# Kernel optimization log

Hardware: AMD Instinct MI355X
Metric: run time of the kernel (lower is better)

Reference implementation:

```python
import jax, jax.numpy as jnp
import numpy as np
from jax import lax

# SLAYER neuron / simulation constants (netParams)
THETA = 1.0      # spike threshold
TAU_SR = 4.0     # PSP (SRM) kernel time constant
TAU_REF = 1.0    # refractory kernel time constant
SCALE_REF = 2.0  # refractory scale (kernel amplitude = -scaleRef*theta)
TAU_RHO = 1.0    # surrogate-gradient width (used in bwd only)
SCALE_RHO = 1.0

B, F_IN, T = 8, 6300, 500  # 6300 = 50*63*2
HID, OUT = 32, 20


def _alpha_scan(x, d):
    """Causal conv with alpha kernel k*d**k along last (time) axis via 2-state recurrence.
    x: [..., T]. y[t] = sum_{j<=t} x[j]*(t-j)*d**(t-j)."""
    xt = jnp.moveaxis(x, -1, 0)  # [T, ...]
    zero = jnp.zeros_like(xt[0])

    def step(carry, xi):
        z, y = carry
        y_new = d * (y + z)       # y[t] = d*(y[t-1] + z[t-1])
        z_new = d * z + xi        # z[t] = d*z[t-1] + x[t]
        return (z_new, y_new), y_new

    _, ys = lax.scan(step, (zero, zero), xt)
    return jnp.moveaxis(ys, 0, -1)


def psp(x):
    """SLAYER psp: convolve spike train with SRM kernel eps(k) = (k/tauSr)*exp(1-k/tauSr)."""
    d = float(np.exp(-1.0 / TAU_SR))
    return jnp.float32(np.e / TAU_SR) * _alpha_scan(x, d)


def _spike_impl(p):
    """Iterative threshold + refractory. p: [..., T] membrane input (post-psp, post-dense).
    Refractory kernel: ref(k) = -scaleRef*theta*(k/tauRef)*exp(1-k/tauRef), realized by the
    same 2-state alpha recurrence driven by emitted spikes."""
    d = float(np.exp(-1.0 / TAU_REF))
    C = jnp.float32(-SCALE_REF * THETA * np.e / TAU_REF)
    pt = jnp.moveaxis(p, -1, 0)  # [T, ...]
    zero = jnp.zeros_like(pt[0])

    def step(carry, pi):
        z, y = carry
        y_new = d * (y + z)                 # alpha state from past spikes (lag>=1)
        u = pi + C * y_new                  # membrane potential incl. refractory
        s = (u >= THETA).astype(pi.dtype)   # hard threshold
        z_new = d * z + s
        return (z_new, y_new), s

    _, ss = lax.scan(step, (zero, zero), pt)
    return jnp.moveaxis(ss, 0, -1)


def spike(p):
    return _spike_impl(p)


def setup_inputs() -> dict:
    key = jax.random.key(0)
    k1, k2, k3 = jax.random.split(key, 3)
    downsampled = (jax.random.uniform(k1, (B, F_IN, T)) < 0.05).astype(jnp.float32)
    w1 = jax.random.normal(k2, (HID, F_IN), jnp.float32) * 0.05
    w2 = jax.random.normal(k3, (OUT, HID), jnp.float32) * 0.3
    return {"downsampled": downsampled, "w1": w1, "w2": w2}


def reference(downsampled, w1, w2):
    # spike_1 = spike(psp(downsampled))
    s1 = spike(psp(downsampled))
    # spike_2 = spike(fc1(psp(spike_1)))
    s2 = spike(jnp.einsum('of,bft->bot', w1, psp(s1)))
    # spike_3 = spike(fc2(psp(spike_2)))
    s3 = spike(jnp.einsum('of,bft->bot', w2, psp(s2)))
    return s3
```

## Files before the change

### kernel.cpp

```cpp
#include <hip/hip_runtime.h>
#include <stdint.h>

#define NB 8
#define F_IN 6300
#define NT 500
#define HID 32
#define NOUT 20
#define NW 99
#define NWD 8

#define D_SR   0.7788007830714049f
#define S_SR   0.6795704571147613f
#define D_REF  0.36787944117144233f
#define C_REF  -5.43656365691809f

#define NROWB ((NB * F_IN) / 4)

__global__ __launch_bounds__(256) void k0_pack(const float* __restrict__ x,
                                               const float* __restrict__ w1,
                                               uint64_t* __restrict__ xb,
                                               float* __restrict__ w1t) {
  const int bid = blockIdx.x;
  const int tid = threadIdx.x;
  if (bid < NROWB) {
    const int row = bid * 4 + (tid >> 6);
    const int lane = tid & 63;
    const float* xr = x + (size_t)row * NT;
    uint64_t m[8];
#pragma unroll
    for (int k = 0; k < 8; k++) {
      int t = k * 64 + lane;
      float v = (t < NT) ? xr[t] : 0.f;
      m[k] = __ballot(v > 0.5f);
    }
    if (lane == 0) {
      uint64_t* dst = xb + (size_t)row * NWD;
#pragma unroll
      for (int k = 0; k < 8; k++) dst[k] = m[k];
    }
    return;
  }
  __shared__ float tl[64][33];
  const int f0 = (bid - NROWB) * 64;
  const int r = tid & 63, g = tid >> 6;
#pragma unroll
  for (int oo = 0; oo < 32; oo += 4) {
    int o = oo + g;
    int f = f0 + r;
    tl[r][o] = (f < F_IN) ? w1[o * F_IN + f] : 0.f;
  }
  __syncthreads();
#pragma unroll
  for (int k = 0; k < 8; k++) {
    int idx = k * 256 + tid;
    int rr = idx >> 5, cc = idx & 31;
    int f = f0 + rr;
    if (f < F_IN) w1t[(size_t)f * 32 + cc] = tl[rr][cc];
  }
}

__global__ __launch_bounds__(64, 1) void k1_layer1(const uint64_t* __restrict__ xb,
                                                   uint64_t* __restrict__ masks) {
  const int wi = blockIdx.x;
  const int b  = blockIdx.y;
  const int lane = threadIdx.x;
  const int f = wi * 64 + lane;
  const uint64_t vmask = __ballot(f < F_IN);
  const int fc = (f < F_IN) ? f : (F_IN - 1);
  const uint64_t* xr = xb + ((size_t)b * F_IN + fc) * NWD;
  uint64_t* mrow = masks + ((size_t)b * NW + wi) * NT;

  float y1 = 0.f, z1 = 0.f, yr = 0.f, zr = 0.f;
  uint64_t wcur = xr[0];

#pragma unroll 1
  for (int gg = 0; gg < 8; gg++) {
    const int gn = (gg < 7) ? gg + 1 : 7;
    uint64_t wnxt = xr[gn];
    const uint32_t wlo = (uint32_t)wcur;
    const uint32_t whi = (uint32_t)(wcur >> 32);
    uint64_t keep = 0;
#pragma unroll
    for (int j = 0; j < 64; j++) {
      const uint32_t bw = (j < 32) ? wlo : whi;
      const bool xbit = ((bw >> (j & 31)) & 1u) != 0u;
      float zm = __fmul_rn(D_SR, z1);
      y1 = __fmul_rn(D_SR, __fadd_rn(y1, z1));
      z1 = xbit ? __fadd_rn(zm, 1.0f) : zm;
      float p = __fmul_rn(S_SR, y1);
      yr = __fmul_rn(D_REF, __fadd_rn(yr, zr));
      float u = __fadd_rn(p, __fmul_rn(C_REF, yr));
      bool s = (u >= 1.0f);
      float zrm = __fmul_rn(D_REF, zr);
      zr = s ? __fadd_rn(zrm, 1.0f) : zrm;
      uint64_t mball = __ballot(s);
      if (lane == j) keep = mball;
    }
    uint64_t* mp = mrow + gg * 64;
    if (gg < 7)                 mp[lane] = keep & vmask;
    else if (lane < NT - 7*64)  mp[lane] = keep & vmask;
    wcur = wnxt;
  }
}

__global__ __launch_bounds__(512) void k2_fc1(const float* __restrict__ w1t,
                                              const uint64_t* __restrict__ masks,
                                              double* __restrict__ R) {
  __shared__ double part[8][32];
  const int tid = threadIdx.x;
  const int wv = tid >> 6;
  const int lane = tid & 63;
  const int half = lane >> 5;
  const int o = lane & 31;
  const int b = blockIdx.x;
  const int t = blockIdx.y * 4 + (wv & 3);
  const int seg = wv >> 2;
  const int wbeg = seg * 50, wend = seg ? NW : 50;
  const uint64_t* mbase = masks + (size_t)b * NW * NT + t;
  const char* wrow = (const char*)w1t + o * 4;
  double acc0 = 0.0, acc1 = 0.0, acc2 = 0.0, acc3 = 0.0;

  int wi = wbeg + half;
  uint64_t mcur = (wi < wend) ? mbase[(size_t)wi * NT] : 0;
  for (; wi < wend; wi += 2) {
    uint64_t mnext = (wi + 2 < wend) ? mbase[(size_t)(wi + 2) * NT] : 0;
    const uint32_t base0 = ((uint32_t)wi << 13);
    uint32_t w = (uint32_t)mcur;
    uint32_t boff = base0;
#pragma unroll
    for (int sub = 0; sub < 2; sub++) {
      while (w) {
        uint32_t i0 = __builtin_ctz(w);                 uint32_t w1_ = w & (w - 1);
        uint32_t i1 = w1_ ? __builtin_ctz(w1_) : 0u;    uint32_t w2_ = w1_ ? (w1_ & (w1_ - 1)) : 0u;
        uint32_t i2 = w2_ ? __builtin_ctz(w2_) : 0u;    uint32_t w3_ = w2_ ? (w2_ & (w2_ - 1)) : 0u;
        uint32_t i3 = w3_ ? __builtin_ctz(w3_) : 0u;    w = w3_ ? (w3_ & (w3_ - 1)) : 0u;
        float a0 = *(const float*)(wrow + boff + (i0 << 7));
        float a1 = *(const float*)(wrow + boff + (i1 << 7));
        float a2 = *(const float*)(wrow + boff + (i2 << 7));
        float a3 = *(const float*)(wrow + boff + (i3 << 7));
        a1 = w1_ ? a1 : 0.0f;
        a2 = w2_ ? a2 : 0.0f;
        a3 = w3_ ? a3 : 0.0f;
        acc0 += (double)a0;
        acc1 += (double)a1;
        acc2 += (double)a2;
        acc3 += (double)a3;
      }
      w = (uint32_t)(mcur >> 32);
      boff = base0 + (32u << 7);
    }
    mcur = mnext;
  }
  double acc = (acc0 + acc1) + (acc2 + acc3);
  int hi2 = __shfl_xor(__double2hiint(acc), 32);
  int lo2 = __shfl_xor(__double2loint(acc), 32);
  acc += __hiloint2double(hi2, lo2);
  if (half == 0) part[wv][o] = acc;
  __syncthreads();
  if (wv < 4 && half == 0) {
    double tot = part[wv][o] + part[wv + 4][o];
    R[((size_t)b * NT + t) * HID + o] = tot;
  }
}

#define SNN_FAST_STEP(rin, EMIT)                                                \
  {                                                                             \
    y2 = __builtin_fma(dsr, y2, w);                                   \
    z2 = __builtin_fma(dsr, z2, (rin));                               \
    w  = dsr * z2;                                                              \
    double p  = ssr * y2;                                                       \
    double u0 = __builtin_fma(cr, q, p);                                        \
    double u1 = u0 + K;                                                         \
    double u  = sp ? u1 : u0;                                                   \
    bool s = (u >= 1.0);                                                        \
    double yr = q + (sp ? dre : 0.0);                                 \
    double zr = zrd + (sp ? 1.0 : 0.0);                           \
    zrd = dre * zr;                                                             \
    q = __builtin_fma(dre, yr, dre * zrd);                             \
    sp = s;                                                                     \
    EMIT                                                                        \
  }

#define K3_GROUP(g, v0, v1, v2, v3)                                             \
  {                                                                             \
    const int t = (g) * 4;                                                      \
    SNN_FAST_STEP(v0, { uint64_t m = __ballot(s);                               \
      if (lane == 0)  m0[t] = (uint32_t)m;                                      \
      if (lane == 32) m1[t] = (uint32_t)(m >> 32); })                           \
    SNN_FAST_STEP(v1, { uint64_t m = __ballot(s);                               \
      if (lane == 0)  m0[t + 1] = (uint32_t)m;                                  \
      if (lane == 32) m1[t + 1] = (uint32_t)(m >> 32); })                       \
    SNN_FAST_STEP(v2, { uint64_t m = __ballot(s);                               \
      if (lane == 0)  m0[t + 2] = (uint32_t)m;                                  \
      if (lane == 32) m1[t + 2] = (uint32_t)(m >> 32); })                       \
    SNN_FAST_STEP(v3, { uint64_t m = __ballot(s);                               \
      if (lane == 0)  m0[t + 3] = (uint32_t)m;                                  \
      if (lane == 32) m1[t + 3] = (uint32_t)(m >> 32); })                       \
  }

__global__ __launch_bounds__(64, 1) void k3_spike2(const double* __restrict__ R,
                                                   uint32_t* __restrict__ s2m) {
  const int blk = blockIdx.x;
  const int lane = threadIdx.x;
  const int half = lane >> 5;
  const int b = blk * 2 + half;
  const int h = lane & 31;
  const double* Rb = R + (size_t)b * NT * HID + h;
  uint32_t* m0 = s2m + (size_t)(blk * 2) * NT;
  uint32_t* m1 = s2m + (size_t)(blk * 2 + 1) * NT;

  const double dsr = (double)D_SR, ssr = (double)S_SR;
  const double dre = (double)D_REF, cr = (double)C_REF;
  const double K = cr * dre;
  double y2 = 0, z2 = 0, w = 0, q = 0, zrd = 0;
  bool sp = false;

  double buf[8][4];
#pragma unroll
  for (int j = 0; j < 8; j++)
#pragma unroll
    for (int e = 0; e < 4; e++) buf[j][e] = Rb[(size_t)(j * 4 + e) * HID];

#pragma unroll 1
  for (int g8 = 0; g8 < 15; g8++) {
#pragma unroll
    for (int j = 0; j < 8; j++) {
      const int g = g8 * 8 + j;
      double v0 = buf[j][0], v1 = buf[j][1], v2 = buf[j][2], v3 = buf[j][3];
      int gp = g + 8;
      if (gp > 124) gp = 124;
#pragma unroll
      for (int e = 0; e < 4; e++) buf[j][e] = Rb[((size_t)gp * 4 + e) * HID];
      K3_GROUP(g, v0, v1, v2, v3)
    }
  }
#pragma unroll
  for (int j = 0; j < 5; j++) {
    const int g = 120 + j;
    double v0 = buf[j][0], v1 = buf[j][1], v2 = buf[j][2], v3 = buf[j][3];
    K3_GROUP(g, v0, v1, v2, v3)
  }
}

__global__ __launch_bounds__(256) void k4_fc2(const float* __restrict__ w2,
                                              const uint32_t* __restrict__ s2m,
                                              double* __restrict__ R3) {
  __shared__ float w2l[NOUT * 33];
  const int tid = threadIdx.x;
  for (int i = tid; i < NOUT * HID; i += 256) w2l[(i >> 5) * 33 + (i & 31)] = w2[i];
  __syncthreads();
  int id = blockIdx.x * 256 + tid;
  if (id >= NB * NOUT * NT) return;
  int o = id % NOUT;
  int rem = id / NOUT;
  int t = rem % NT;
  int b = rem / NT;
  uint32_t m = s2m[(size_t)b * NT + t];
  const float* wr = w2l + o * 33;
  double acc = 0.0;
  while (m) {
    uint32_t i0 = __builtin_ctz(m);                 uint32_t m1_ = m & (m - 1);
    uint32_t i1 = m1_ ? __builtin_ctz(m1_) : 0u;    uint32_t m2_ = m1_ ? (m1_ & (m1_ - 1)) : 0u;
    uint32_t i2 = m2_ ? __builtin_ctz(m2_) : 0u;    uint32_t m3_ = m2_ ? (m2_ & (m2_ - 1)) : 0u;
    uint32_t i3 = m3_ ? __builtin_ctz(m3_) : 0u;    m = m3_ ? (m3_ & (m3_ - 1)) : 0u;
    float a0 = wr[i0];
    float a1 = m1_ ? wr[i1] : 0.0f;
    float a2 = m2_ ? wr[i2] : 0.0f;
    float a3 = m3_ ? wr[i3] : 0.0f;
    acc += (double)a0;
    acc += (double)a1;
    acc += (double)a2;
    acc += (double)a3;
  }
  R3[id] = acc;
}

#define K5_GROUP(g, v0, v1, v2, v3)                                             \
  {                                                                             \
    float4 ov;                                                                  \
    SNN_FAST_STEP(v0, { ov.x = s ? 1.0f : 0.0f; })                              \
    SNN_FAST_STEP(v1, { ov.y = s ? 1.0f : 0.0f; })                              \
    SNN_FAST_STEP(v2, { ov.z = s ? 1.0f : 0.0f; })                              \
    SNN_FAST_STEP(v3, { ov.w = s ? 1.0f : 0.0f; })                              \
    *(float4*)(orow + (g) * 4) = ov;                                            \
  }

__global__ __launch_bounds__(64, 1) void k5_out(const double* __restrict__ R3,
                                                float* __restrict__ out) {
  int id = blockIdx.x * 64 + threadIdx.x;
  if (id >= NB * NOUT) return;
  const int b = id / NOUT;
  const int o = id % NOUT;
  const double* Rb = R3 + (size_t)b * NT * NOUT + o;
  float* orow = out + (size_t)id * NT;

  const double dsr = (double)D_SR, ssr = (double)S_SR;
  const double dre = (double)D_REF, cr = (double)C_REF;
  const double K = cr * dre;
  double y2 = 0, z2 = 0, w = 0, q = 0, zrd = 0;
  bool sp = false;

  double buf[8][4];
#pragma unroll
  for (int j = 0; j < 8; j++)
#pragma unroll
    for (int e = 0; e < 4; e++) buf[j][e] = Rb[(size_t)(j * 4 + e) * NOUT];

#pragma unroll 1
  for (int g8 = 0; g8 < 15; g8++) {
#pragma unroll
    for (int j = 0; j < 8; j++) {
      const int g = g8 * 8 + j;
      double v0 = buf[j][0], v1 = buf[j][1], v2 = buf[j][2], v3 = buf[j][3];
      int gp = g + 8;
      if (gp > 124) gp = 124;
#pragma unroll
      for (int e = 0; e < 4; e++) buf[j][e] = Rb[((size_t)gp * 4 + e) * NOUT];
      K5_GROUP(g, v0, v1, v2, v3)
    }
  }
#pragma unroll
  for (int j = 0; j < 5; j++) {
    const int g = 120 + j;
    double v0 = buf[j][0], v1 = buf[j][1], v2 = buf[j][2], v3 = buf[j][3];
    K5_GROUP(g, v0, v1, v2, v3)
  }
}

extern "C" void kernel_launch(void* const* d_in, const int* in_sizes, int n_in,
                              void* d_out, int out_size, void* d_ws, size_t ws_size,
                              hipStream_t stream) {
  const float* x  = (const float*)d_in[0];
  const float* w1 = (const float*)d_in[1];
  const float* w2 = (const float*)d_in[2];
  float* out = (float*)d_out;

  uint8_t* ws = (uint8_t*)d_ws;
  const size_t W1T_BYTES  = (size_t)F_IN * HID * 4;
  const size_t XBF_BYTES  = (size_t)NB * F_IN * NWD * 8;
  const size_t MASK_BYTES = (size_t)NB * NW * NT * 8;
  const size_t R_BYTES    = (size_t)NB * HID * NT * 8;
  const size_t S2M_BYTES  = (size_t)NB * NT * 4;
  float*    w1t   = (float*)ws;
  uint64_t* xbF   = (uint64_t*)(ws + W1T_BYTES);
  uint64_t* masks = (uint64_t*)(ws + W1T_BYTES + XBF_BYTES);
  double*   R     = (double*)(ws + W1T_BYTES + XBF_BYTES + MASK_BYTES);
  uint32_t* s2m   = (uint32_t*)(ws + W1T_BYTES + XBF_BYTES + MASK_BYTES + R_BYTES);
  double*   R3    = (double*)(ws + W1T_BYTES + XBF_BYTES + MASK_BYTES + R_BYTES + S2M_BYTES);

  k0_pack<<<NROWB + 99, 256, 0, stream>>>(x, w1, xbF, w1t);
  k1_layer1<<<dim3(NW, NB), 64, 0, stream>>>(xbF, masks);
  k2_fc1<<<dim3(NB, NT / 4), 512, 0, stream>>>(w1t, masks, R);
  k3_spike2<<<4, 64, 0, stream>>>(R, s2m);
  k4_fc2<<<(NB * NOUT * NT + 255) / 256, 256, 0, stream>>>(w2, s2m, R3);
  k5_out<<<3, 64, 0, stream>>>(R3, out);
}
```

Before: 302.9 us.

## Fuse layer-2 spike, fc2, and output spike kernels into one per-batch block

Merges the spike2 scan, fc2 sparse accumulation and final spike scan into a single kernel with one 512-thread block per batch. Intermediate spike masks and fc2 results stay in shared memory instead of global memory, which removes two kernel launches and their global round trips. The cost is that each block's serial scans use only 32 or 20 lanes while the other waves sit idle at barriers. Only 8 blocks run, and each spike2 scan now occupies half a wave instead of sharing a wave between two batches.

```diff
diff --git a/kernel.cpp b/kernel.cpp
--- a/kernel.cpp
+++ b/kernel.cpp
@@ -181,101 +181,20 @@
     EMIT                                                                        \
   }
 
-#define K3_GROUP(g, v0, v1, v2, v3)                                             \
+#define P1_GROUP(g, v0, v1, v2, v3)                                             \
   {                                                                             \
     const int t = (g) * 4;                                                      \
-    SNN_FAST_STEP(v0, { uint64_t m = __ballot(s);                               \
-      if (lane == 0)  m0[t] = (uint32_t)m;                                      \
-      if (lane == 32) m1[t] = (uint32_t)(m >> 32); })                           \
-    SNN_FAST_STEP(v1, { uint64_t m = __ballot(s);                               \
-      if (lane == 0)  m0[t + 1] = (uint32_t)m;                                  \
-      if (lane == 32) m1[t + 1] = (uint32_t)(m >> 32); })                       \
-    SNN_FAST_STEP(v2, { uint64_t m = __ballot(s);                               \
-      if (lane == 0)  m0[t + 2] = (uint32_t)m;                                  \
-      if (lane == 32) m1[t + 2] = (uint32_t)(m >> 32); })                       \
-    SNN_FAST_STEP(v3, { uint64_t m = __ballot(s);                               \
-      if (lane == 0)  m0[t + 3] = (uint32_t)m;                                  \
-      if (lane == 32) m1[t + 3] = (uint32_t)(m >> 32); })                       \
-  }
-
-__global__ __launch_bounds__(64, 1) void k3_spike2(const double* __restrict__ R,
-                                                   uint32_t* __restrict__ s2m) {
-  const int blk = blockIdx.x;
-  const int lane = threadIdx.x;
-  const int half = lane >> 5;
-  const int b = blk * 2 + half;
-  const int h = lane & 31;
-  const double* Rb = R + (size_t)b * NT * HID + h;
-  uint32_t* m0 = s2m + (size_t)(blk * 2) * NT;
-  uint32_t* m1 = s2m + (size_t)(blk * 2 + 1) * NT;
-
-  const double dsr = (double)D_SR, ssr = (double)S_SR;
-  const double dre = (double)D_REF, cr = (double)C_REF;
-  const double K = cr * dre;
-  double y2 = 0, z2 = 0, w = 0, q = 0, zrd = 0;
-  bool sp = false;
-
-  double buf[8][4];
-#pragma unroll
-  for (int j = 0; j < 8; j++)
-#pragma unroll
-    for (int e = 0; e < 4; e++) buf[j][e] = Rb[(size_t)(j * 4 + e) * HID];
-
-#pragma unroll 1
-  for (int g8 = 0; g8 < 15; g8++) {
-#pragma unroll
-    for (int j = 0; j < 8; j++) {
-      const int g = g8 * 8 + j;
-      double v0 = buf[j][0], v1 = buf[j][1], v2 = buf[j][2], v3 = buf[j][3];
-      int gp = g + 8;
-      if (gp > 124) gp = 124;
-#pragma unroll
-      for (int e = 0; e < 4; e++) buf[j][e] = Rb[((size_t)gp * 4 + e) * HID];
-      K3_GROUP(g, v0, v1, v2, v3)
-    }
-  }
-#pragma unroll
-  for (int j = 0; j < 5; j++) {
-    const int g = 120 + j;
-    double v0 = buf[j][0], v1 = buf[j][1], v2 = buf[j][2], v3 = buf[j][3];
-    K3_GROUP(g, v0, v1, v2, v3)
-  }
-}
-
-__global__ __launch_bounds__(256) void k4_fc2(const float* __restrict__ w2,
-                                              const uint32_t* __restrict__ s2m,
-                                              double* __restrict__ R3) {
-  __shared__ float w2l[NOUT * 33];
-  const int tid = threadIdx.x;
-  for (int i = tid; i < NOUT * HID; i += 256) w2l[(i >> 5) * 33 + (i & 31)] = w2[i];
-  __syncthreads();
-  int id = blockIdx.x * 256 + tid;
-  if (id >= NB * NOUT * NT) return;
-  int o = id % NOUT;
-  int rem = id / NOUT;
-  int t = rem % NT;
-  int b = rem / NT;
-  uint32_t m = s2m[(size_t)b * NT + t];
-  const float* wr = w2l + o * 33;
-  double acc = 0.0;
-  while (m) {
-    uint32_t i0 = __builtin_ctz(m);                 uint32_t m1_ = m & (m - 1);
-    uint32_t i1 = m1_ ? __builtin_ctz(m1_) : 0u;    uint32_t m2_ = m1_ ? (m1_ & (m1_ - 1)) : 0u;
-    uint32_t i2 = m2_ ? __builtin_ctz(m2_) : 0u;    uint32_t m3_ = m2_ ? (m2_ & (m2_ - 1)) : 0u;
-    uint32_t i3 = m3_ ? __builtin_ctz(m3_) : 0u;    m = m3_ ? (m3_ & (m3_ - 1)) : 0u;
-    float a0 = wr[i0];
-    float a1 = m1_ ? wr[i1] : 0.0f;
-    float a2 = m2_ ? wr[i2] : 0.0f;
-    float a3 = m3_ ? wr[i3] : 0.0f;
-    acc += (double)a0;
-    acc += (double)a1;
-    acc += (double)a2;
-    acc += (double)a3;
-  }
-  R3[id] = acc;
-}
-
-#define K5_GROUP(g, v0, v1, v2, v3)                                             \
+    SNN_FAST_STEP(v0, { uint32_t mm = (uint32_t)__ballot(s);                    \
+      if (lane == 0) s2l[t] = mm; })                                            \
+    SNN_FAST_STEP(v1, { uint32_t mm = (uint32_t)__ballot(s);                    \
+      if (lane == 0) s2l[t + 1] = mm; })                                        \
+    SNN_FAST_STEP(v2, { uint32_t mm = (uint32_t)__ballot(s);                    \
+      if (lane == 0) s2l[t + 2] = mm; })                                        \
+    SNN_FAST_STEP(v3, { uint32_t mm = (uint32_t)__ballot(s);                    \
+      if (lane == 0) s2l[t + 3] = mm; })                                        \
+  }
+
+#define P3_GROUP(g, v0, v1, v2, v3)                                             \
   {                                                                             \
     float4 ov;                                                                  \
     SNN_FAST_STEP(v0, { ov.x = s ? 1.0f : 0.0f; })                              \
@@ -285,45 +204,102 @@
     *(float4*)(orow + (g) * 4) = ov;                                            \
   }
 
-__global__ __launch_bounds__(64, 1) void k5_out(const double* __restrict__ R3,
-                                                float* __restrict__ out) {
-  int id = blockIdx.x * 64 + threadIdx.x;
-  if (id >= NB * NOUT) return;
-  const int b = id / NOUT;
-  const int o = id % NOUT;
-  const double* Rb = R3 + (size_t)b * NT * NOUT + o;
-  float* orow = out + (size_t)id * NT;
+__global__ __launch_bounds__(512, 1) void k345(const float* __restrict__ w2,
+                                               const double* __restrict__ R,
+                                               float* __restrict__ out) {
+  __shared__ float    w2l[NOUT * 33];
+  __shared__ uint32_t s2l[NT];
+  __shared__ double   r3l[NT * NOUT];
+  const int b = blockIdx.x;
+  const int tid = threadIdx.x;
+  const int lane = tid & 63;
+  const int wv = tid >> 6;
+
+  for (int i = tid; i < NOUT * HID; i += 512) w2l[(i >> 5) * 33 + (i & 31)] = w2[i];
 
   const double dsr = (double)D_SR, ssr = (double)S_SR;
   const double dre = (double)D_REF, cr = (double)C_REF;
   const double K = cr * dre;
-  double y2 = 0, z2 = 0, w = 0, q = 0, zrd = 0;
-  bool sp = false;
-
-  double buf[8][4];
-#pragma unroll
-  for (int j = 0; j < 8; j++)
-#pragma unroll
-    for (int e = 0; e < 4; e++) buf[j][e] = Rb[(size_t)(j * 4 + e) * NOUT];
+
+  if (wv == 0 && lane < 32) {
+    const double* Rb = R + (size_t)b * NT * HID + lane;
+    double y2 = 0, z2 = 0, w = 0, q = 0, zrd = 0;
+    bool sp = false;
+
+    double buf[8][4];
+#pragma unroll
+    for (int j = 0; j < 8; j++)
+#pragma unroll
+      for (int e = 0; e < 4; e++) buf[j][e] = Rb[(size_t)(j * 4 + e) * HID];
 
 #pragma unroll 1
-  for (int g8 = 0; g8 < 15; g8++) {
-#pragma unroll
-    for (int j = 0; j < 8; j++) {
-      const int g = g8 * 8 + j;
+    for (int g8 = 0; g8 < 15; g8++) {
+#pragma unroll
+      for (int j = 0; j < 8; j++) {
+        const int g = g8 * 8 + j;
+        double v0 = buf[j][0], v1 = buf[j][1], v2 = buf[j][2], v3 = buf[j][3];
+        int gp = g + 8;
+        if (gp > 124) gp = 124;
+#pragma unroll
+        for (int e = 0; e < 4; e++) buf[j][e] = Rb[((size_t)gp * 4 + e) * HID];
+        P1_GROUP(g, v0, v1, v2, v3)
+      }
+    }
+#pragma unroll
+    for (int j = 0; j < 5; j++) {
+      const int g = 120 + j;
       double v0 = buf[j][0], v1 = buf[j][1], v2 = buf[j][2], v3 = buf[j][3];
-      int gp = g + 8;
-      if (gp > 124) gp = 124;
-#pragma unroll
-      for (int e = 0; e < 4; e++) buf[j][e] = Rb[((size_t)gp * 4 + e) * NOUT];
-      K5_GROUP(g, v0, v1, v2, v3)
-    }
-  }
-#pragma unroll
-  for (int j = 0; j < 5; j++) {
-    const int g = 120 + j;
-    double v0 = buf[j][0], v1 = buf[j][1], v2 = buf[j][2], v3 = buf[j][3];
-    K5_GROUP(g, v0, v1, v2, v3)
+      P1_GROUP(g, v0, v1, v2, v3)
+    }
+  }
+  __syncthreads();
+
+#pragma unroll 1
+  for (int base = 0; base < NT * NOUT; base += 512) {
+    int task = base + tid;
+    if (task < NT * NOUT) {
+      int o = task % NOUT;
+      int t = task / NOUT;
+      uint32_t m = s2l[t];
+      const float* wr = w2l + o * 33;
+      double acc = 0.0;
+      while (m) {
+        uint32_t i0 = __builtin_ctz(m);                 uint32_t m1_ = m & (m - 1);
+        uint32_t i1 = m1_ ? __builtin_ctz(m1_) : 0u;    uint32_t m2_ = m1_ ? (m1_ & (m1_ - 1)) : 0u;
+        uint32_t i2 = m2_ ? __builtin_ctz(m2_) : 0u;    uint32_t m3_ = m2_ ? (m2_ & (m2_ - 1)) : 0u;
+        uint32_t i3 = m3_ ? __builtin_ctz(m3_) : 0u;    m = m3_ ? (m3_ & (m3_ - 1)) : 0u;
+        float a0 = wr[i0];
+        float a1 = m1_ ? wr[i1] : 0.0f;
+        float a2 = m2_ ? wr[i2] : 0.0f;
+        float a3 = m3_ ? wr[i3] : 0.0f;
+        acc += (double)a0;
+        acc += (double)a1;
+        acc += (double)a2;
+        acc += (double)a3;
+      }
+      r3l[t * NOUT + o] = acc;
+    }
+  }
+  __syncthreads();
+
+  if (wv == 0 && lane < NOUT) {
+    const int o = lane;
+    float* orow = out + ((size_t)b * NOUT + o) * NT;
+    double y2 = 0, z2 = 0, w = 0, q = 0, zrd = 0;
+    bool sp = false;
+
+    double c0 = r3l[0 * NOUT + o], c1 = r3l[1 * NOUT + o];
+    double c2 = r3l[2 * NOUT + o], c3 = r3l[3 * NOUT + o];
+#pragma unroll 1
+    for (int g = 0; g < 125; g++) {
+      const int gp = (g < 124) ? g + 1 : 124;
+      double n0 = r3l[(gp * 4 + 0) * NOUT + o];
+      double n1 = r3l[(gp * 4 + 1) * NOUT + o];
+      double n2 = r3l[(gp * 4 + 2) * NOUT + o];
+      double n3 = r3l[(gp * 4 + 3) * NOUT + o];
+      P3_GROUP(g, c0, c1, c2, c3)
+      c0 = n0; c1 = n1; c2 = n2; c3 = n3;
+    }
   }
 }
 
@@ -339,19 +315,13 @@
   const size_t W1T_BYTES  = (size_t)F_IN * HID * 4;
   const size_t XBF_BYTES  = (size_t)NB * F_IN * NWD * 8;
   const size_t MASK_BYTES = (size_t)NB * NW * NT * 8;
-  const size_t R_BYTES    = (size_t)NB * HID * NT * 8;
-  const size_t S2M_BYTES  = (size_t)NB * NT * 4;
   float*    w1t   = (float*)ws;
   uint64_t* xbF   = (uint64_t*)(ws + W1T_BYTES);
   uint64_t* masks = (uint64_t*)(ws + W1T_BYTES + XBF_BYTES);
   double*   R     = (double*)(ws + W1T_BYTES + XBF_BYTES + MASK_BYTES);
-  uint32_t* s2m   = (uint32_t*)(ws + W1T_BYTES + XBF_BYTES + MASK_BYTES + R_BYTES);
-  double*   R3    = (double*)(ws + W1T_BYTES + XBF_BYTES + MASK_BYTES + R_BYTES + S2M_BYTES);
 
   k0_pack<<<NROWB + 99, 256, 0, stream>>>(x, w1, xbF, w1t);
   k1_layer1<<<dim3(NW, NB), 64, 0, stream>>>(xbF, masks);
   k2_fc1<<<dim3(NB, NT / 4), 512, 0, stream>>>(w1t, masks, R);
-  k3_spike2<<<4, 64, 0, stream>>>(R, s2m);
-  k4_fc2<<<(NB * NOUT * NT + 255) / 256, 256, 0, stream>>>(w2, s2m, R3);
-  k5_out<<<3, 64, 0, stream>>>(R3, out);
-}
+  k345<<<NB, 512, 0, stream>>>(w2, R, out);
+}
```

Result: slower. 310.5 us (+2.5%).
